# Performance work log

Hardware: AMD Instinct MI355X
Metric: run time of the kernel (lower is better)

Reference implementation:

```python
import jax, jax.numpy as jnp
import numpy as np

MAX_K = 16
CLUSTER_ITERS = 3
TEMP = 0.8
EPS = 1e-6


def setup_inputs() -> dict:
    key = jax.random.key(0)
    k1, k2 = jax.random.split(key, 2)
    B, C, H, W = 4, 256, 128, 128
    embeddings = jax.random.normal(k1, (B, C, H, W), dtype=jnp.float32)
    # 1x1 conv == per-pixel linear: weight [max_k, C], bias [max_k]
    seed_w = jax.random.normal(k2, (MAX_K, C), dtype=jnp.float32) * 0.05
    seed_b = jnp.zeros((MAX_K,), dtype=jnp.float32)
    return {"embeddings": embeddings, "seed_w": seed_w, "seed_b": seed_b, "k": 8}


def reference(embeddings, seed_w, seed_b, k):
    b, c, h, w = embeddings.shape
    n = h * w
    feats = embeddings.reshape(b, c, n)                     # [b,c,n]

    # seed_proj (1x1 conv) restricted to first k output channels
    seeds = jnp.einsum('oc,bcn->bon', seed_w[:k], feats) + seed_b[:k][None, :, None]
    assign = jax.nn.softmax(seeds, axis=1)                  # [b,k,n]
    proto = jnp.einsum('bkn,bcn->bkc', assign, feats) / (assign.sum(axis=2)[..., None] + EPS)

    # ||f||^2 is constant across iterations
    f_sq = jnp.sum(feats * feats, axis=1)                   # [b,n]

    logits = None
    for _ in range(CLUSTER_ITERS):                          # small fixed iter count
        p_sq = jnp.sum(proto * proto, axis=2)               # [b,k]
        cross = jnp.einsum('bkc,bcn->bkn', proto, feats)    # [b,k,n]
        # squared L2 distance via matmul trick (same math as (f-p)^2 sum over c)
        dist = f_sq[:, None, :] + p_sq[:, :, None] - 2.0 * cross
        logits = -dist / TEMP                               # [b,k,n]
        assign = jax.nn.softmax(logits, axis=1)
        denom = assign.sum(axis=2, keepdims=True) + EPS     # [b,k,1]
        proto = jnp.einsum('bkn,bcn->bkc', assign, feats) / denom

    logits_map = logits.reshape(b, k, h, w)
    probs = jax.nn.softmax(logits_map, axis=1)
    # bilinear upsample x4, align_corners=False (half-pixel) == jax 'linear' resize
    probs_full = jax.image.resize(probs, (b, k, 4 * h, 4 * w), method='linear')
    return probs_full, proto, logits_map
```

## Files before the change

kernel.cpp:

```cpp
#include <hip/hip_runtime.h>
#include <hip/hip_bf16.h>
#include <math.h>

#define BB   4
#define CCH  256
#define KK   8
#define NPIX 16384
#define TILE 64
#define NBLK 256
#define TEMP_INV 1.25f
#define EPSF 1e-6f

__device__ __forceinline__ float bf_lo(unsigned int u) { return __uint_as_float(u << 16); }
__device__ __forceinline__ float bf_hi(unsigned int u) { return __uint_as_float(u & 0xffff0000u); }

template<int MODE>
__global__ __launch_bounds__(512, 6)
void skm_pass(const float* __restrict__ feats,
              const float* __restrict__ seed_w,
              const float* __restrict__ seed_b,
              const float* __restrict__ proto_t,
              const float* __restrict__ psq_part,
              float* __restrict__ fsq,
              float* __restrict__ part_num,
              float* __restrict__ part_den,
              float* __restrict__ logits_out,
              float* __restrict__ probs_out)
{
    __shared__ unsigned int fb_s[CCH][32];
    __shared__ float cross_s[8][KK][66];
    __shared__ float w_s[KK][68];
    __shared__ float aux_s[8][TILE];

    const int t   = threadIdx.x;
    const int bid = blockIdx.x;
    const int b   = bid >> 8;
    const int blk = bid & 255;
    const int n0  = blk * TILE;

    const int p  = t & 63;
    const int g  = t >> 6;
    const int c0 = __builtin_amdgcn_readfirstlane(g) * 32;
    const float* fcol = feats + (size_t)b * CCH * NPIX + (size_t)c0 * NPIX + n0 + p;
    const float* pt   = proto_t + (size_t)b * CCH * KK + (size_t)c0 * KK;

    float cr[KK];
    #pragma unroll
    for (int k = 0; k < KK; ++k) cr[k] = 0.f;
    float fs = 0.f;

    #pragma unroll 8
    for (int cc = 0; cc < 32; ++cc) {
        const float f = fcol[(size_t)cc * NPIX];
        if (MODE == 0) fs = fmaf(f, f, fs);
        const int c  = c0 + cc;
        const int wp = (p >> 1) ^ ((c & 15) << 1);
        ((__hip_bfloat16*)fb_s)[(c << 6) + (wp << 1) + (p & 1)] = __float2bfloat16(f);
        if (MODE == 0) {
            #pragma unroll
            for (int k = 0; k < KK; ++k)
                cr[k] = fmaf(seed_w[k * CCH + c], f, cr[k]);
        } else {
            const float* pr = pt + cc * KK;
            #pragma unroll
            for (int k = 0; k < KK; ++k)
                cr[k] = fmaf(pr[k], f, cr[k]);
        }
    }
    #pragma unroll
    for (int k = 0; k < KK; ++k) cross_s[g][k][p] = cr[k];
    if (MODE == 0) aux_s[g][p] = fs;
    __syncthreads();

    {
        const int pp = t >> 3, k = t & 7;
        float lg = 0.f;
        #pragma unroll
        for (int gg = 0; gg < 8; ++gg) lg += cross_s[gg][k][pp];
        if (MODE == 0) {
            lg += seed_b[k];
            if (k == 0) {
                float fv = 0.f;
                #pragma unroll
                for (int gg = 0; gg < 8; ++gg) fv += aux_s[gg][pp];
                fsq[b * NPIX + n0 + pp] = fv;
            }
        } else {
            const float4 q0 = ((const float4*)psq_part)[(b * KK + k) * 2];
            const float4 q1 = ((const float4*)psq_part)[(b * KK + k) * 2 + 1];
            const float pk = ((q0.x + q0.y) + (q0.z + q0.w))
                           + ((q1.x + q1.y) + (q1.z + q1.w));
            if (MODE == 2) {
                const float fv = fsq[b * NPIX + n0 + pp];
                lg = (2.f * lg - fv - pk) * TEMP_INV;
            } else {
                lg = fmaf(2.f * TEMP_INV, lg, -TEMP_INV * pk);
            }
        }
        float m = lg;
        m = fmaxf(m, __shfl_xor(m, 1, 64));
        m = fmaxf(m, __shfl_xor(m, 2, 64));
        m = fmaxf(m, __shfl_xor(m, 4, 64));
        const float e = expf(lg - m);
        float ssum = e;
        ssum += __shfl_xor(ssum, 1, 64);
        ssum += __shfl_xor(ssum, 2, 64);
        ssum += __shfl_xor(ssum, 4, 64);
        const float wv = e / ssum;
        w_s[k][pp] = wv;
        if (MODE == 2) aux_s[k][pp] = lg;
    }
    __syncthreads();

    if (MODE == 2) {
        const int k2 = t >> 6, p2 = t & 63;
        logits_out[((size_t)b * KK + k2) * NPIX + n0 + p2] = aux_s[k2][p2];
        probs_out [((size_t)b * KK + k2) * NPIX + n0 + p2] = w_s[k2][p2];
    }

    if (t < 256) {
        const int kk = t >> 5, ll = t & 31;
        float s = w_s[kk][2 * ll] + w_s[kk][2 * ll + 1];
        s += __shfl_xor(s, 16, 64);
        s += __shfl_xor(s, 8, 64);
        s += __shfl_xor(s, 4, 64);
        s += __shfl_xor(s, 2, 64);
        s += __shfl_xor(s, 1, 64);
        if (ll == 0) part_den[(b * NBLK + blk) * KK + kk] = s;
    }

    {
        const int c = t & 255, h = t >> 8;
        const int s2 = (c & 15) << 1;
        const uint2* row2 = (const uint2*)fb_s[c];
        float accx[KK], accy[KK];
        #pragma unroll
        for (int k = 0; k < KK; ++k) { accx[k] = 0.f; accy[k] = 0.f; }
        #pragma unroll
        for (int j = 0; j < 8; ++j) {
            const uint2 u = row2[((16 * h + 2 * j) ^ s2) >> 1];
            const float f0 = bf_lo(u.x), f1 = bf_hi(u.x);
            const float f2 = bf_lo(u.y), f3 = bf_hi(u.y);
            const int px = 32 * h + 4 * j;
            #pragma unroll
            for (int k = 0; k < KK; ++k) {
                const float4 w4 = *(const float4*)&w_s[k][px];
                accx[k] = fmaf(f2, w4.z, fmaf(f0, w4.x, accx[k]));
                accy[k] = fmaf(f3, w4.w, fmaf(f1, w4.y, accy[k]));
            }
        }
        float (*acc_s)[KK][CCH] = (float (*)[KK][CCH])cross_s;
        #pragma unroll
        for (int k = 0; k < KK; ++k) acc_s[h][k][c] = accx[k] + accy[k];
        __syncthreads();
        #pragma unroll
        for (int u2 = t; u2 < KK * CCH; u2 += 512) {
            const int k = u2 >> 8, c2 = u2 & 255;
            part_num[(((size_t)b * NBLK + blk) * KK + k) * CCH + c2] =
                acc_s[0][k][c2] + acc_s[1][k][c2];
        }
    }
}

template<bool FINAL>
__global__ __launch_bounds__(512)
void skm_reduce(const float* __restrict__ part_num,
                const float* __restrict__ part_den,
                float* __restrict__ proto_t,
                float* __restrict__ psq_part,
                float* __restrict__ proto_out,
                const float* __restrict__ probs_ws,
                float* __restrict__ probs_full)
{
    const int bid = blockIdx.x;
    if (FINAL && bid >= 256) {
        const int gid = (bid - 256) * 512 + threadIdx.x;
        const int jb = gid & 127;
        const int i  = (gid >> 7) & 511;
        const int bk = gid >> 16;
        const float* src = probs_ws + (size_t)bk * NPIX;
        const float y   = i * 0.25f - 0.375f;
        const float y0f = floorf(y);
        const float fy  = y - y0f;
        const int   y0  = (int)y0f;
        const int ya = min(max(y0, 0), 127);
        const int yb = min(max(y0 + 1, 0), 127);
        const int xm = max(jb - 1, 0);
        const int xp = min(jb + 1, 127);
        const float* r0 = src + ya * 128;
        const float* r1 = src + yb * 128;
        const float wy0 = 1.f - fy;
        const float am = r0[xm] * wy0 + r1[xm] * fy;
        const float ac = r0[jb] * wy0 + r1[jb] * fy;
        const float ap = r0[xp] * wy0 + r1[xp] * fy;
        float4 o;
        o.x = 0.375f * am + 0.625f * ac;
        o.y = 0.125f * am + 0.875f * ac;
        o.z = 0.875f * ac + 0.125f * ap;
        o.w = 0.625f * ac + 0.375f * ap;
        ((float4*)probs_full)[gid] = o;
        return;
    }

    const int cq = bid & 7;
    const int bk = bid >> 3;
    const int b = bk >> 3, k = bk & 7;
    const int t = threadIdx.x;

    __shared__ float red[16][32];
    __shared__ float den_s[4];

    float dv = (t < 256) ? part_den[(b * NBLK + t) * KK + k] : 0.f;
    dv += __shfl_xor(dv, 32, 64);
    dv += __shfl_xor(dv, 16, 64);
    dv += __shfl_xor(dv, 8, 64);
    dv += __shfl_xor(dv, 4, 64);
    dv += __shfl_xor(dv, 2, 64);
    dv += __shfl_xor(dv, 1, 64);
    if (t < 256 && (t & 63) == 0) den_s[t >> 6] = dv;

    const int jj = t >> 5, cl = t & 31;
    const int c = cq * 32 + cl;
    float s = 0.f;
    #pragma unroll 4
    for (int j = 0; j < 16; ++j)
        s += part_num[(((size_t)b * NBLK + jj * 16 + j) * KK + k) * CCH + c];
    red[jj][cl] = s;
    __syncthreads();

    if (t < 32) {
        const float den = den_s[0] + den_s[1] + den_s[2] + den_s[3] + EPSF;
        float pv = 0.f;
        #pragma unroll
        for (int j2 = 0; j2 < 16; ++j2) pv += red[j2][t];
        pv /= den;
        const int c2 = cq * 32 + t;
        proto_t[((size_t)b * CCH + c2) * KK + k] = pv;
        if (proto_out) proto_out[(b * KK + k) * CCH + c2] = pv;
        float q = pv * pv;
        q += __shfl_xor(q, 16, 64);
        q += __shfl_xor(q, 8, 64);
        q += __shfl_xor(q, 4, 64);
        q += __shfl_xor(q, 2, 64);
        q += __shfl_xor(q, 1, 64);
        if (t == 0) psq_part[(b * KK + k) * 8 + cq] = q;
    }
}

extern "C" void kernel_launch(void* const* d_in, const int* in_sizes, int n_in,
                              void* d_out, int out_size, void* d_ws, size_t ws_size,
                              hipStream_t stream)
{
    const float* feats  = (const float*)d_in[0];
    const float* seed_w = (const float*)d_in[1];
    const float* seed_b = (const float*)d_in[2];

    float* out        = (float*)d_out;
    float* probs_full = out;
    float* proto_out  = out + 8388608;
    float* logits_out = out + 8388608 + 8192;

    float* ws       = (float*)d_ws;
    float* fsq      = ws;
    float* part_den = ws + 65536;
    float* proto_t  = part_den + 8192;
    float* psq_part = proto_t + 8192;
    float* probs_ws = psq_part + 256;
    float* part_num = probs_ws + 524288;

    const dim3 pg(BB * NBLK), pb(512);
    const dim3 rg(256), rb(512);

    skm_pass<0><<<pg, pb, 0, stream>>>(feats, seed_w, seed_b, proto_t, psq_part,
                                       fsq, part_num, part_den, nullptr, nullptr);
    skm_reduce<false><<<rg, rb, 0, stream>>>(part_num, part_den, proto_t, psq_part,
                                             nullptr, probs_ws, probs_full);
    skm_pass<1><<<pg, pb, 0, stream>>>(feats, seed_w, seed_b, proto_t, psq_part,
                                       fsq, part_num, part_den, nullptr, nullptr);
    skm_reduce<false><<<rg, rb, 0, stream>>>(part_num, part_den, proto_t, psq_part,
                                             nullptr, probs_ws, probs_full);
    skm_pass<1><<<pg, pb, 0, stream>>>(feats, seed_w, seed_b, proto_t, psq_part,
                                       fsq, part_num, part_den, nullptr, nullptr);
    skm_reduce<false><<<rg, rb, 0, stream>>>(part_num, part_den, proto_t, psq_part,
                                             nullptr, probs_ws, probs_full);
    skm_pass<2><<<pg, pb, 0, stream>>>(feats, seed_w, seed_b, proto_t, psq_part,
                                       fsq, part_num, part_den, logits_out, probs_ws);
    skm_reduce<true><<<dim3(256 + 4096), rb, 0, stream>>>(part_num, part_den, proto_t, psq_part,
                                                          proto_out, probs_ws, probs_full);
}
```

Before: 97.93 us.

## Restructure skm_pass: stage bf16 prototypes in LDS, shuffle-reduce cross terms, split k

The pass kernel now loads the seed weights or prototypes once per block into LDS as packed bf16, so each thread reads eight weights with one 128-bit LDS load instead of eight scalar global loads. Thread mapping changes so the eight channel groups for a pixel share a wavefront, and cross terms are reduced with shuffles rather than through an LDS buffer and an extra barrier. Softmax is computed per thread across all k. The numerator accumulation splits k across thread halves instead of pixels, which removes the final LDS reduction and barrier. Occupancy hint goes to 8, and the bf16 rounding of prototypes adds precision loss in the logits.

```diff
diff --git a/kernel.cpp b/kernel.cpp
--- a/kernel.cpp
+++ b/kernel.cpp
@@ -13,9 +13,16 @@
 
 __device__ __forceinline__ float bf_lo(unsigned int u) { return __uint_as_float(u << 16); }
 __device__ __forceinline__ float bf_hi(unsigned int u) { return __uint_as_float(u & 0xffff0000u); }
+__device__ __forceinline__ unsigned short bfbits(float f) {
+    __hip_bfloat16 h = __float2bfloat16(f);
+    return *reinterpret_cast<unsigned short*>(&h);
+}
+__device__ __forceinline__ unsigned int pack_bf2(float a, float b) {
+    return (unsigned int)bfbits(a) | ((unsigned int)bfbits(b) << 16);
+}
 
 template<int MODE>
-__global__ __launch_bounds__(512, 6)
+__global__ __launch_bounds__(512, 8)
 void skm_pass(const float* __restrict__ feats,
               const float* __restrict__ seed_w,
               const float* __restrict__ seed_b,
@@ -28,9 +35,9 @@
               float* __restrict__ probs_out)
 {
     __shared__ unsigned int fb_s[CCH][32];
-    __shared__ float cross_s[8][KK][66];
+    __shared__ unsigned int proto_s[32][8][4];
     __shared__ float w_s[KK][68];
-    __shared__ float aux_s[8][TILE];
+    __shared__ float psq_s[8];
 
     const int t   = threadIdx.x;
     const int bid = blockIdx.x;
@@ -38,11 +45,36 @@
     const int blk = bid & 255;
     const int n0  = blk * TILE;
 
-    const int p  = t & 63;
-    const int g  = t >> 6;
-    const int c0 = __builtin_amdgcn_readfirstlane(g) * 32;
-    const float* fcol = feats + (size_t)b * CCH * NPIX + (size_t)c0 * NPIX + n0 + p;
-    const float* pt   = proto_t + (size_t)b * CCH * KK + (size_t)c0 * KK;
+    {
+        const int c = t >> 1, kh = t & 1;
+        if (MODE == 0) {
+            const float s0 = seed_w[(4 * kh + 0) * CCH + c];
+            const float s1 = seed_w[(4 * kh + 1) * CCH + c];
+            const float s2 = seed_w[(4 * kh + 2) * CCH + c];
+            const float s3 = seed_w[(4 * kh + 3) * CCH + c];
+            proto_s[c & 31][c >> 5][2 * kh]     = pack_bf2(s0, s1);
+            proto_s[c & 31][c >> 5][2 * kh + 1] = pack_bf2(s2, s3);
+            if (t < 8) psq_s[t] = seed_b[t];
+        } else {
+            const float4 pv = ((const float4*)(proto_t + (size_t)b * CCH * KK))[t];
+            proto_s[c & 31][c >> 5][2 * kh]     = pack_bf2(pv.x, pv.y);
+            proto_s[c & 31][c >> 5][2 * kh + 1] = pack_bf2(pv.z, pv.w);
+            if (t < 8) {
+                const float4 q0 = ((const float4*)psq_part)[(b * KK + t) * 2];
+                const float4 q1 = ((const float4*)psq_part)[(b * KK + t) * 2 + 1];
+                psq_s[t] = -TEMP_INV * (((q0.x + q0.y) + (q0.z + q0.w))
+                                      + ((q1.x + q1.y) + (q1.z + q1.w)));
+            }
+        }
+    }
+    __syncthreads();
+
+    const int lane = t & 63;
+    const int g    = t >> 6;
+    const int px   = (g << 3) + (lane & 7);
+    const int cgrp = lane >> 3;
+    const int c0   = cgrp << 5;
+    const float* fcol = feats + ((size_t)b * CCH + c0) * NPIX + n0 + px;
 
     float cr[KK];
     #pragma unroll
@@ -54,69 +86,60 @@
         const float f = fcol[(size_t)cc * NPIX];
         if (MODE == 0) fs = fmaf(f, f, fs);
         const int c  = c0 + cc;
-        const int wp = (p >> 1) ^ ((c & 15) << 1);
-        ((__hip_bfloat16*)fb_s)[(c << 6) + (wp << 1) + (p & 1)] = __float2bfloat16(f);
-        if (MODE == 0) {
-            #pragma unroll
-            for (int k = 0; k < KK; ++k)
-                cr[k] = fmaf(seed_w[k * CCH + c], f, cr[k]);
-        } else {
-            const float* pr = pt + cc * KK;
-            #pragma unroll
-            for (int k = 0; k < KK; ++k)
-                cr[k] = fmaf(pr[k], f, cr[k]);
+        const int wp = (px >> 1) ^ ((((c & 15) ^ (c >> 5))) << 1);
+        ((unsigned short*)fb_s)[(c << 6) + (wp << 1) + (px & 1)] = bfbits(f);
+        const uint4 pv = *(const uint4*)&proto_s[cc][cgrp][0];
+        cr[0] = fmaf(bf_lo(pv.x), f, cr[0]);
+        cr[1] = fmaf(bf_hi(pv.x), f, cr[1]);
+        cr[2] = fmaf(bf_lo(pv.y), f, cr[2]);
+        cr[3] = fmaf(bf_hi(pv.y), f, cr[3]);
+        cr[4] = fmaf(bf_lo(pv.z), f, cr[4]);
+        cr[5] = fmaf(bf_hi(pv.z), f, cr[5]);
+        cr[6] = fmaf(bf_lo(pv.w), f, cr[6]);
+        cr[7] = fmaf(bf_hi(pv.w), f, cr[7]);
+    }
+    #pragma unroll
+    for (int k = 0; k < KK; ++k) {
+        cr[k] += __shfl_xor(cr[k], 8, 64);
+        cr[k] += __shfl_xor(cr[k], 16, 64);
+        cr[k] += __shfl_xor(cr[k], 32, 64);
+    }
+    if (MODE == 0) {
+        fs += __shfl_xor(fs, 8, 64);
+        fs += __shfl_xor(fs, 16, 64);
+        fs += __shfl_xor(fs, 32, 64);
+        if (cgrp == 0) fsq[b * NPIX + n0 + px] = fs;
+    }
+
+    {
+        float fvt = 0.f;
+        if (MODE == 2) fvt = -TEMP_INV * fsq[b * NPIX + n0 + px];
+        float lg[KK];
+        #pragma unroll
+        for (int k = 0; k < KK; ++k) {
+            if (MODE == 0)      lg[k] = cr[k] + psq_s[k];
+            else if (MODE == 1) lg[k] = fmaf(2.f * TEMP_INV, cr[k], psq_s[k]);
+            else                lg[k] = fmaf(2.f * TEMP_INV, cr[k], psq_s[k] + fvt);
         }
-    }
-    #pragma unroll
-    for (int k = 0; k < KK; ++k) cross_s[g][k][p] = cr[k];
-    if (MODE == 0) aux_s[g][p] = fs;
+        float m = lg[0];
+        #pragma unroll
+        for (int k = 1; k < KK; ++k) m = fmaxf(m, lg[k]);
+        float e[KK], ssum = 0.f;
+        #pragma unroll
+        for (int k = 0; k < KK; ++k) { e[k] = expf(lg[k] - m); ssum += e[k]; }
+        const float inv = 1.f / ssum;
+        float wv = e[0], lgo = lg[0];
+        #pragma unroll
+        for (int k = 1; k < KK; ++k)
+            if (cgrp == k) { wv = e[k]; lgo = lg[k]; }
+        wv *= inv;
+        w_s[cgrp][px] = wv;
+        if (MODE == 2) {
+            logits_out[((size_t)b * KK + cgrp) * NPIX + n0 + px] = lgo;
+            probs_out [((size_t)b * KK + cgrp) * NPIX + n0 + px] = wv;
+        }
+    }
     __syncthreads();
-
-    {
-        const int pp = t >> 3, k = t & 7;
-        float lg = 0.f;
-        #pragma unroll
-        for (int gg = 0; gg < 8; ++gg) lg += cross_s[gg][k][pp];
-        if (MODE == 0) {
-            lg += seed_b[k];
-            if (k == 0) {
-                float fv = 0.f;
-                #pragma unroll
-                for (int gg = 0; gg < 8; ++gg) fv += aux_s[gg][pp];
-                fsq[b * NPIX + n0 + pp] = fv;
-            }
-        } else {
-            const float4 q0 = ((const float4*)psq_part)[(b * KK + k) * 2];
-            const float4 q1 = ((const float4*)psq_part)[(b * KK + k) * 2 + 1];
-            const float pk = ((q0.x + q0.y) + (q0.z + q0.w))
-                           + ((q1.x + q1.y) + (q1.z + q1.w));
-            if (MODE == 2) {
-                const float fv = fsq[b * NPIX + n0 + pp];
-                lg = (2.f * lg - fv - pk) * TEMP_INV;
-            } else {
-                lg = fmaf(2.f * TEMP_INV, lg, -TEMP_INV * pk);
-            }
-        }
-        float m = lg;
-        m = fmaxf(m, __shfl_xor(m, 1, 64));
-        m = fmaxf(m, __shfl_xor(m, 2, 64));
-        m = fmaxf(m, __shfl_xor(m, 4, 64));
-        const float e = expf(lg - m);
-        float ssum = e;
-        ssum += __shfl_xor(ssum, 1, 64);
-        ssum += __shfl_xor(ssum, 2, 64);
-        ssum += __shfl_xor(ssum, 4, 64);
-        const float wv = e / ssum;
-        w_s[k][pp] = wv;
-        if (MODE == 2) aux_s[k][pp] = lg;
-    }
-    __syncthreads();
-
-    if (MODE == 2) {
-        const int k2 = t >> 6, p2 = t & 63;
-        logits_out[((size_t)b * KK + k2) * NPIX + n0 + p2] = aux_s[k2][p2];
-        probs_out [((size_t)b * KK + k2) * NPIX + n0 + p2] = w_s[k2][p2];
-    }
 
     if (t < 256) {
         const int kk = t >> 5, ll = t & 31;
@@ -130,35 +153,29 @@
     }
 
     {
-        const int c = t & 255, h = t >> 8;
-        const int s2 = (c & 15) << 1;
+        const int c  = t & 255, kh = t >> 8;
+        const int sw = (c & 15) ^ (c >> 5);
         const uint2* row2 = (const uint2*)fb_s[c];
-        float accx[KK], accy[KK];
-        #pragma unroll
-        for (int k = 0; k < KK; ++k) { accx[k] = 0.f; accy[k] = 0.f; }
-        #pragma unroll
-        for (int j = 0; j < 8; ++j) {
-            const uint2 u = row2[((16 * h + 2 * j) ^ s2) >> 1];
+        const int kb = kh * 4;
+        float acc[4];
+        #pragma unroll
+        for (int kk2 = 0; kk2 < 4; ++kk2) acc[kk2] = 0.f;
+        #pragma unroll
+        for (int j = 0; j < 16; ++j) {
+            const uint2 u = row2[j ^ sw];
             const float f0 = bf_lo(u.x), f1 = bf_hi(u.x);
             const float f2 = bf_lo(u.y), f3 = bf_hi(u.y);
-            const int px = 32 * h + 4 * j;
+            const int pxj = 4 * j;
             #pragma unroll
-            for (int k = 0; k < KK; ++k) {
-                const float4 w4 = *(const float4*)&w_s[k][px];
-                accx[k] = fmaf(f2, w4.z, fmaf(f0, w4.x, accx[k]));
-                accy[k] = fmaf(f3, w4.w, fmaf(f1, w4.y, accy[k]));
+            for (int kk2 = 0; kk2 < 4; ++kk2) {
+                const float4 w4 = *(const float4*)&w_s[kb + kk2][pxj];
+                acc[kk2] = fmaf(f3, w4.w, fmaf(f2, w4.z,
+                           fmaf(f1, w4.y, fmaf(f0, w4.x, acc[kk2]))));
             }
         }
-        float (*acc_s)[KK][CCH] = (float (*)[KK][CCH])cross_s;
-        #pragma unroll
-        for (int k = 0; k < KK; ++k) acc_s[h][k][c] = accx[k] + accy[k];
-        __syncthreads();
-        #pragma unroll
-        for (int u2 = t; u2 < KK * CCH; u2 += 512) {
-            const int k = u2 >> 8, c2 = u2 & 255;
-            part_num[(((size_t)b * NBLK + blk) * KK + k) * CCH + c2] =
-                acc_s[0][k][c2] + acc_s[1][k][c2];
-        }
+        #pragma unroll
+        for (int kk2 = 0; kk2 < 4; ++kk2)
+            part_num[(((size_t)b * NBLK + blk) * KK + (kb + kk2)) * CCH + c] = acc[kk2];
     }
 }
 
```

Result: slower. 117.4 us (+19.8%).

## Cut LDS footprint in iteration passes to raise occupancy and split accumulation by cluster

Applied to the files above, without the earlier changes.

The iteration passes (MODE 1/2) now reduce the partial cross products through a smaller bf16 scratch buffer, in two phases, instead of an fp32 8-way buffer. This shrinks LDS use and lets launch bounds request 8 waves instead of 6. The prototype accumulation now splits work by cluster halves rather than pixel halves, so each thread writes its part_num values directly and the extra LDS reduction and barrier are gone. The feature swizzle was also changed. Rounding the cross terms to bf16 lowers logit precision and adds a barrier.

```diff
diff --git a/kernel.cpp b/kernel.cpp
--- a/kernel.cpp
+++ b/kernel.cpp
@@ -13,9 +13,16 @@
 
 __device__ __forceinline__ float bf_lo(unsigned int u) { return __uint_as_float(u << 16); }
 __device__ __forceinline__ float bf_hi(unsigned int u) { return __uint_as_float(u & 0xffff0000u); }
+__device__ __forceinline__ unsigned short bfbits(float f) {
+    __hip_bfloat16 h = __float2bfloat16(f);
+    return *reinterpret_cast<unsigned short*>(&h);
+}
+__device__ __forceinline__ float us2f(unsigned short u) {
+    return __uint_as_float((unsigned int)u << 16);
+}
 
 template<int MODE>
-__global__ __launch_bounds__(512, 6)
+__global__ __launch_bounds__(512, (MODE == 0) ? 6 : 8)
 void skm_pass(const float* __restrict__ feats,
               const float* __restrict__ seed_w,
               const float* __restrict__ seed_b,
@@ -28,9 +35,14 @@
               float* __restrict__ probs_out)
 {
     __shared__ unsigned int fb_s[CCH][32];
-    __shared__ float cross_s[8][KK][66];
     __shared__ float w_s[KK][68];
-    __shared__ float aux_s[8][TILE];
+    constexpr int XBYTES = (MODE == 0) ? (8 * KK * 66 * 4 + 8 * TILE * 4)
+                                       : (4 * KK * 66 * 2);
+    __shared__ __align__(16) unsigned char xmem[XBYTES];
+    float (*cross_f)[KK][66] = (float (*)[KK][66])xmem;
+    float (*aux)[TILE] = (float (*)[TILE])(xmem + 8 * KK * 66 * 4);
+    unsigned short (*cross_h)[KK][66] = (unsigned short (*)[KK][66])xmem;
+    float (*lgst)[66] = (float (*)[66])xmem;
 
     const int t   = threadIdx.x;
     const int bid = blockIdx.x;
@@ -54,8 +66,8 @@
         const float f = fcol[(size_t)cc * NPIX];
         if (MODE == 0) fs = fmaf(f, f, fs);
         const int c  = c0 + cc;
-        const int wp = (p >> 1) ^ ((c & 15) << 1);
-        ((__hip_bfloat16*)fb_s)[(c << 6) + (wp << 1) + (p & 1)] = __float2bfloat16(f);
+        const int wp = (p >> 1) ^ ((((c & 15) ^ ((c >> 4) & 3))) << 1);
+        ((unsigned short*)fb_s)[(c << 6) + (wp << 1) + (p & 1)] = bfbits(f);
         if (MODE == 0) {
             #pragma unroll
             for (int k = 0; k < KK; ++k)
@@ -67,25 +79,42 @@
                 cr[k] = fmaf(pr[k], f, cr[k]);
         }
     }
-    #pragma unroll
-    for (int k = 0; k < KK; ++k) cross_s[g][k][p] = cr[k];
-    if (MODE == 0) aux_s[g][p] = fs;
-    __syncthreads();
+
+    if (MODE == 0) {
+        #pragma unroll
+        for (int k = 0; k < KK; ++k) cross_f[g][k][p] = cr[k];
+        aux[g][p] = fs;
+        __syncthreads();
+    } else {
+        if (g < 4) {
+            #pragma unroll
+            for (int k = 0; k < KK; ++k) cross_h[g][k][p] = bfbits(cr[k]);
+        }
+        __syncthreads();
+        if (g >= 4) {
+            #pragma unroll
+            for (int k = 0; k < KK; ++k)
+                cross_h[g - 4][k][p] = bfbits(us2f(cross_h[g - 4][k][p]) + cr[k]);
+        }
+        __syncthreads();
+    }
 
     {
         const int pp = t >> 3, k = t & 7;
         float lg = 0.f;
-        #pragma unroll
-        for (int gg = 0; gg < 8; ++gg) lg += cross_s[gg][k][pp];
         if (MODE == 0) {
+            #pragma unroll
+            for (int gg = 0; gg < 8; ++gg) lg += cross_f[gg][k][pp];
             lg += seed_b[k];
             if (k == 0) {
                 float fv = 0.f;
                 #pragma unroll
-                for (int gg = 0; gg < 8; ++gg) fv += aux_s[gg][pp];
+                for (int gg = 0; gg < 8; ++gg) fv += aux[gg][pp];
                 fsq[b * NPIX + n0 + pp] = fv;
             }
         } else {
+            #pragma unroll
+            for (int gg = 0; gg < 4; ++gg) lg += us2f(cross_h[gg][k][pp]);
             const float4 q0 = ((const float4*)psq_part)[(b * KK + k) * 2];
             const float4 q1 = ((const float4*)psq_part)[(b * KK + k) * 2 + 1];
             const float pk = ((q0.x + q0.y) + (q0.z + q0.w))
@@ -107,14 +136,17 @@
         ssum += __shfl_xor(ssum, 2, 64);
         ssum += __shfl_xor(ssum, 4, 64);
         const float wv = e / ssum;
+        if (MODE == 2) {
+            __syncthreads();
+            lgst[k][pp] = lg;
+        }
         w_s[k][pp] = wv;
-        if (MODE == 2) aux_s[k][pp] = lg;
     }
     __syncthreads();
 
     if (MODE == 2) {
         const int k2 = t >> 6, p2 = t & 63;
-        logits_out[((size_t)b * KK + k2) * NPIX + n0 + p2] = aux_s[k2][p2];
+        logits_out[((size_t)b * KK + k2) * NPIX + n0 + p2] = lgst[k2][p2];
         probs_out [((size_t)b * KK + k2) * NPIX + n0 + p2] = w_s[k2][p2];
     }
 
@@ -130,35 +162,29 @@
     }
 
     {
-        const int c = t & 255, h = t >> 8;
-        const int s2 = (c & 15) << 1;
+        const int c  = t & 255, kh = t >> 8;
+        const int sw = (c & 15) ^ ((c >> 4) & 3);
         const uint2* row2 = (const uint2*)fb_s[c];
-        float accx[KK], accy[KK];
-        #pragma unroll
-        for (int k = 0; k < KK; ++k) { accx[k] = 0.f; accy[k] = 0.f; }
-        #pragma unroll
-        for (int j = 0; j < 8; ++j) {
-            const uint2 u = row2[((16 * h + 2 * j) ^ s2) >> 1];
+        const int kb = kh * 4;
+        float acc[4];
+        #pragma unroll
+        for (int kk2 = 0; kk2 < 4; ++kk2) acc[kk2] = 0.f;
+        #pragma unroll
+        for (int j = 0; j < 16; ++j) {
+            const uint2 u = row2[j ^ sw];
             const float f0 = bf_lo(u.x), f1 = bf_hi(u.x);
             const float f2 = bf_lo(u.y), f3 = bf_hi(u.y);
-            const int px = 32 * h + 4 * j;
-            #pragma unroll
-            for (int k = 0; k < KK; ++k) {
-                const float4 w4 = *(const float4*)&w_s[k][px];
-                accx[k] = fmaf(f2, w4.z, fmaf(f0, w4.x, accx[k]));
-                accy[k] = fmaf(f3, w4.w, fmaf(f1, w4.y, accy[k]));
+            const int pxj = 4 * j;
+            #pragma unroll
+            for (int kk2 = 0; kk2 < 4; ++kk2) {
+                const float4 w4 = *(const float4*)&w_s[kb + kk2][pxj];
+                acc[kk2] = fmaf(f3, w4.w, fmaf(f2, w4.z,
+                           fmaf(f1, w4.y, fmaf(f0, w4.x, acc[kk2]))));
             }
         }
-        float (*acc_s)[KK][CCH] = (float (*)[KK][CCH])cross_s;
-        #pragma unroll
-        for (int k = 0; k < KK; ++k) acc_s[h][k][c] = accx[k] + accy[k];
-        __syncthreads();
-        #pragma unroll
-        for (int u2 = t; u2 < KK * CCH; u2 += 512) {
-            const int k = u2 >> 8, c2 = u2 & 255;
-            part_num[(((size_t)b * NBLK + blk) * KK + k) * CCH + c2] =
-                acc_s[0][k][c2] + acc_s[1][k][c2];
-        }
+        #pragma unroll
+        for (int kk2 = 0; kk2 < 4; ++kk2)
+            part_num[(((size_t)b * NBLK + blk) * KK + (kb + kk2)) * CCH + c] = acc[kk2];
     }
 }
 
```

New measurement: 118.8 us. 1.21x slower.
